# Kernel tuning notes

Hardware: AMD Instinct MI355X
Metric: run time of the kernel (lower is better)

## Reference

```python
import jax, jax.numpy as jnp
import numpy as np

NEG_NUM = -10000.0

def setup_inputs() -> dict:
    key = jax.random.key(0)
    k1, k2, k3, k4, k5, k6 = jax.random.split(key, 6)
    batch, enc_len = 32, 2048
    ctx_size, query_size, att_hid = 1024, 1024, 512
    in_dim = ctx_size + query_size
    ctx = jax.random.normal(k1, (batch, enc_len, ctx_size), dtype=jnp.float32)
    query = jax.random.normal(k2, (batch, query_size), dtype=jnp.float32)
    mask = jax.random.randint(k3, (batch, enc_len), 0, 2, dtype=jnp.int32)
    # Linear params (stored as (in, out) for x @ W + b)
    s1 = 1.0 / np.sqrt(in_dim)
    W1 = jax.random.uniform(k4, (in_dim, att_hid), jnp.float32, -s1, s1)
    b1 = jnp.zeros((att_hid,), jnp.float32)
    s2 = 1.0 / np.sqrt(att_hid)
    W2 = jax.random.uniform(k5, (att_hid, 1), jnp.float32, -s2, s2)
    b2 = jnp.zeros((1,), jnp.float32)
    return {"ctx": ctx, "query": query, "W1": W1, "b1": b1, "W2": W2, "b2": b2, "mask": mask}

def reference(ctx, query, W1, b1, W2, b2, mask):
    # ctx: (B, S, Dc), query: (B, Dq)
    B, S, Dc = ctx.shape
    Dq = query.shape[-1]
    # Equivalent to concat([ctx, query_expanded]) @ W1: split W1 into ctx/query blocks
    Wc, Wq = W1[:Dc], W1[Dc:]
    hidden = jnp.tanh(jnp.einsum('bsd,dh->bsh', ctx, Wc)
                      + (query @ Wq)[:, None, :] + b1)      # (B, S, H)
    score = jnp.einsum('bsh,h->bs', hidden, W2[:, 0]) + b2[0]  # (B, S)
    score = jnp.where(mask == 0, NEG_NUM, score)
    p_ctx = jax.nn.softmax(score, axis=-1)                   # (B, S)
    expected_ctx = jnp.einsum('bs,bsd->bd', p_ctx, ctx)      # (B, Dc)
    return (expected_ctx, p_ctx)
```

## Files before the change

kernel.cpp:

```cpp
#include <hip/hip_runtime.h>

typedef __bf16 bf16;
typedef __attribute__((ext_vector_type(8))) __bf16 bf16x8;
typedef __attribute__((ext_vector_type(4))) __bf16 bf16x4;
typedef __attribute__((ext_vector_type(4))) float f32x4;

#define B_  32
#define S_  2048
#define DC  1024
#define DQ  1024
#define H_  512
#define M_  (B_*S_)

#define BM  128
#define BN  512
#define BK  32

#define GLD16(g, l) __builtin_amdgcn_global_load_lds( \
    (__attribute__((address_space(1))) void*)(g),     \
    (__attribute__((address_space(3))) void*)(l), 16, 0, 0)

__global__ __launch_bounds__(256) void k_wconv(const float* __restrict__ W1,
                                               bf16* __restrict__ WcT2) {
    __shared__ bf16 t[32 * 520];
    const int kb = blockIdx.x, tid = threadIdx.x;
    #pragma unroll
    for (int i = 0; i < 16; ++i) {
        int base = (i * 256 + tid) * 4;
        int k = base >> 9;
        int h = base & 511;
        const float4 v = *(const float4*)(W1 + ((size_t)(kb * 32 + k)) * H_ + h);
        bf16x4 pk = { (bf16)v.x, (bf16)v.y, (bf16)v.z, (bf16)v.w };
        *(bf16x4*)(&t[k * 520 + h]) = pk;
    }
    __syncthreads();
    #pragma unroll
    for (int i = 0; i < 16; ++i) {
        int j = (i * 256 + tid) * 4;
        int col = j >> 5;
        int kk  = j & 31;
        bf16x4 o = { t[kk * 520 + col], t[(kk + 1) * 520 + col],
                     t[(kk + 2) * 520 + col], t[(kk + 3) * 520 + col] };
        *(bf16x4*)(WcT2 + (size_t)kb * 16384 + j) = o;
    }
}

__global__ __launch_bounds__(256) void k_qb(const float* __restrict__ query,
                                            const float* __restrict__ W1,
                                            const float* __restrict__ b1,
                                            float* __restrict__ qb) {
    const int hblk = blockIdx.x, b = blockIdx.y, tid = threadIdx.x;
    __shared__ float q[DQ];
    __shared__ float red[256];
    #pragma unroll
    for (int i = 0; i < 4; ++i)
        q[tid + i * 256] = query[(size_t)b * DQ + tid + i * 256];
    __syncthreads();
    const int h  = hblk * 64 + (tid & 63);
    const int kc = tid >> 6;
    const float* w = W1 + (size_t)DC * H_ + (size_t)(kc * 256) * H_ + h;
    const float* qv = q + kc * 256;
    float acc = 0.0f;
    #pragma unroll 8
    for (int k = 0; k < 256; ++k)
        acc = fmaf(qv[k], w[(size_t)k * H_], acc);
    red[tid] = acc;
    __syncthreads();
    if (tid < 64)
        qb[(size_t)b * H_ + hblk * 64 + tid] =
            red[tid] + red[tid + 64] + red[tid + 128] + red[tid + 192] + b1[hblk * 64 + tid];
}

__global__ __launch_bounds__(512, 2) void k_gemm(const float* __restrict__ ctx,
                                                 const bf16*  __restrict__ WcT2,
                                                 const float* __restrict__ qb,
                                                 const float* __restrict__ W2,
                                                 float* __restrict__ score) {
    __shared__ bf16 As[BM * BK];
    __shared__ bf16 Bs[BN * BK];
    __shared__ float qs[BN];
    __shared__ float ws2[BN];
    __shared__ float red[BM * 4];

    const int tid  = threadIdx.x;
    const int mblk = blockIdx.x;
    const size_t row_base = (size_t)mblk * BM;
    const int b = mblk >> 4;

    qs[tid]  = qb[(size_t)b * H_ + tid];
    ws2[tid] = W2[tid];

    const int lane = tid & 63;
    const int wave = tid >> 6;
    const int wm   = wave & 1;
    const int wn   = wave >> 1;
    const int l16  = lane & 15;
    const int quad = lane >> 4;

    f32x4 acc[4][8] = {};

    const int am = tid >> 2;
    const int ak = (tid & 3) << 3;
    const float* actx = ctx + (row_base + am) * (size_t)DC + ak;
    bf16* awr = &As[am * BK + ak];
    const bf16* bsrc = WcT2 + tid * 8;
    bf16* bdst = &Bs[tid * 8];
    const bf16* aP = &As[(wm * 64 + l16) * BK + quad * 8];
    const bf16* bP = &Bs[(wn * 128 + l16) * BK + quad * 8];

    for (int kb = 0; kb < DC / BK; ++kb) {
        #pragma unroll
        for (int i = 0; i < 4; ++i)
            GLD16(bsrc + (size_t)kb * 16384 + i * 4096, bdst + i * 4096);
        const float4 v0 = *(const float4*)(actx + kb * BK);
        const float4 v1 = *(const float4*)(actx + kb * BK + 4);
        bf16x8 a8 = { (bf16)v0.x, (bf16)v0.y, (bf16)v0.z, (bf16)v0.w,
                      (bf16)v1.x, (bf16)v1.y, (bf16)v1.z, (bf16)v1.w };
        *(bf16x8*)awr = a8;
        __syncthreads();

        bf16x8 aF[4], bF[8];
        #pragma unroll
        for (int mf = 0; mf < 4; ++mf) aF[mf] = *(const bf16x8*)(aP + mf * (16 * BK));
        #pragma unroll
        for (int nf = 0; nf < 8; ++nf) bF[nf] = *(const bf16x8*)(bP + nf * (16 * BK));
        #pragma unroll
        for (int mf = 0; mf < 4; ++mf)
            #pragma unroll
            for (int nf = 0; nf < 8; ++nf)
                acc[mf][nf] = __builtin_amdgcn_mfma_f32_16x16x32_bf16(aF[mf], bF[nf], acc[mf][nf], 0, 0, 0);
        __syncthreads();
    }

    float qv[8], wv[8];
    #pragma unroll
    for (int nf = 0; nf < 8; ++nf) {
        int c = wn * 128 + nf * 16 + l16;
        qv[nf] = qs[c];
        wv[nf] = ws2[c];
    }
    #pragma unroll
    for (int mf = 0; mf < 4; ++mf) {
        #pragma unroll
        for (int r = 0; r < 4; ++r) {
            float s = 0.0f;
            #pragma unroll
            for (int nf = 0; nf < 8; ++nf) {
                float x = acc[mf][nf][r] + qv[nf];
                float t = 1.0f - 2.0f / (1.0f + __expf(2.0f * x));
                s = fmaf(t, wv[nf], s);
            }
            s += __shfl_xor(s, 1);
            s += __shfl_xor(s, 2);
            s += __shfl_xor(s, 4);
            s += __shfl_xor(s, 8);
            if (l16 == 0)
                red[(wm * 64 + mf * 16 + quad * 4 + r) * 4 + wn] = s;
        }
    }
    __syncthreads();
    if (tid < BM)
        score[row_base + tid] = red[tid * 4] + red[tid * 4 + 1] + red[tid * 4 + 2] + red[tid * 4 + 3];
}

__global__ __launch_bounds__(256) void k_softmax(const float* __restrict__ score,
                                                 const float* __restrict__ b2,
                                                 const int*   __restrict__ mask,
                                                 float* __restrict__ p_out) {
    int b = blockIdx.x, tid = threadIdx.x;
    __shared__ float red[256];
    float loc[8];
    float b2v = b2[0];
    float mx = -1e30f;
    #pragma unroll
    for (int i = 0; i < 8; ++i) {
        size_t r = (size_t)b * S_ + i * 256 + tid;
        float v = score[r] + b2v;
        if (mask[r] == 0) v = -10000.0f;
        loc[i] = v;
        mx = fmaxf(mx, v);
    }
    red[tid] = mx; __syncthreads();
    for (int o = 128; o > 0; o >>= 1) {
        if (tid < o) red[tid] = fmaxf(red[tid], red[tid + o]);
        __syncthreads();
    }
    mx = red[0]; __syncthreads();
    float se = 0.0f;
    #pragma unroll
    for (int i = 0; i < 8; ++i) {
        float e = __expf(loc[i] - mx);
        loc[i] = e;
        se += e;
    }
    red[tid] = se; __syncthreads();
    for (int o = 128; o > 0; o >>= 1) {
        if (tid < o) red[tid] += red[tid + o];
        __syncthreads();
    }
    float inv = 1.0f / red[0];
    #pragma unroll
    for (int i = 0; i < 8; ++i)
        p_out[(size_t)b * S_ + i * 256 + tid] = loc[i] * inv;
}

__global__ __launch_bounds__(256) void k_expected(const float* __restrict__ ctx,
                                                  const float* __restrict__ p,
                                                  float* __restrict__ partial) {
    int b = blockIdx.x, ch = blockIdx.y, tid = threadIdx.x;
    __shared__ float ps[128];
    if (tid < 128) ps[tid] = p[(size_t)b * S_ + ch * 128 + tid];
    __syncthreads();
    const float* base = ctx + ((size_t)b * S_ + ch * 128) * DC + tid * 4;
    float ax = 0.f, ay = 0.f, az = 0.f, aw = 0.f;
    #pragma unroll 4
    for (int s = 0; s < 128; ++s) {
        const float4 v = *(const float4*)(base + (size_t)s * DC);
        float w = ps[s];
        ax = fmaf(w, v.x, ax);
        ay = fmaf(w, v.y, ay);
        az = fmaf(w, v.z, az);
        aw = fmaf(w, v.w, aw);
    }
    float4 o = { ax, ay, az, aw };
    *(float4*)(partial + ((size_t)(b * 16 + ch)) * DC + tid * 4) = o;
}

__global__ __launch_bounds__(256) void k_reduce(const float* __restrict__ partial,
                                                float* __restrict__ out) {
    int b = blockIdx.x, tid = threadIdx.x;
    float4 acc = { 0.f, 0.f, 0.f, 0.f };
    #pragma unroll
    for (int c = 0; c < 16; ++c) {
        const float4 v = *(const float4*)(partial + ((size_t)(b * 16 + c)) * DC + tid * 4);
        acc.x += v.x; acc.y += v.y; acc.z += v.z; acc.w += v.w;
    }
    *(float4*)(out + (size_t)b * DC + tid * 4) = acc;
}

extern "C" void kernel_launch(void* const* d_in, const int* in_sizes, int n_in,
                              void* d_out, int out_size, void* d_ws, size_t ws_size,
                              hipStream_t stream) {
    (void)in_sizes; (void)n_in; (void)out_size; (void)ws_size;
    const float* ctx   = (const float*)d_in[0];
    const float* query = (const float*)d_in[1];
    const float* W1    = (const float*)d_in[2];
    const float* b1    = (const float*)d_in[3];
    const float* W2    = (const float*)d_in[4];
    const float* b2    = (const float*)d_in[5];
    const int*   mask  = (const int*)d_in[6];

    float* out      = (float*)d_out;
    float* expected = out;
    float* p_out    = out + 32768;

    char* w = (char*)d_ws;
    bf16*  WcT2      = (bf16*)w;
    float* qb        = (float*)(w + (1 << 20));
    float* score     = (float*)(w + (1 << 20) + (64 << 10));
    float* partial_e = (float*)(w + (1 << 20) + (320 << 10));

    k_wconv   <<<32, 256, 0, stream>>>(W1, WcT2);
    k_qb      <<<dim3(8, B_), 256, 0, stream>>>(query, W1, b1, qb);
    k_gemm    <<<512, 512, 0, stream>>>(ctx, WcT2, qb, W2, score);
    k_softmax <<<B_, 256, 0, stream>>>(score, b2, mask, p_out);
    k_expected<<<dim3(B_, 16), 256, 0, stream>>>(ctx, p_out, partial_e);
    k_reduce  <<<B_, 256, 0, stream>>>(partial_e, expected);
}
```

Before: 521.0 us.

## Double-buffer GEMM tiles, merge prep kernels, split expected-ctx into more chunks

The GEMM main loop now double-buffers its A and B LDS tiles, prefetching the next K slice while MFMAs run on the current one, so only one barrier per iteration is needed. The weight conversion and query projection kernels are merged into one finer-grained prep launch. The expected-context pass is split into 32 chunks instead of 16 for more parallelism. Risks: 80KB of LDS per block lowers occupancy (launch bounds drop the min-2 hint), and the reduce step now sums twice as many partials.

```diff
diff --git a/kernel.cpp b/kernel.cpp
--- a/kernel.cpp
+++ b/kernel.cpp
@@ -15,80 +15,78 @@
 #define BM  128
 #define BN  512
 #define BK  32
+#define NCH 32
 
 #define GLD16(g, l) __builtin_amdgcn_global_load_lds( \
     (__attribute__((address_space(1))) void*)(g),     \
     (__attribute__((address_space(3))) void*)(l), 16, 0, 0)
 
-__global__ __launch_bounds__(256) void k_wconv(const float* __restrict__ W1,
-                                               bf16* __restrict__ WcT2) {
-    __shared__ bf16 t[32 * 520];
-    const int kb = blockIdx.x, tid = threadIdx.x;
-    #pragma unroll
-    for (int i = 0; i < 16; ++i) {
-        int base = (i * 256 + tid) * 4;
-        int k = base >> 9;
-        int h = base & 511;
-        const float4 v = *(const float4*)(W1 + ((size_t)(kb * 32 + k)) * H_ + h);
-        bf16x4 pk = { (bf16)v.x, (bf16)v.y, (bf16)v.z, (bf16)v.w };
-        *(bf16x4*)(&t[k * 520 + h]) = pk;
-    }
-    __syncthreads();
-    #pragma unroll
-    for (int i = 0; i < 16; ++i) {
-        int j = (i * 256 + tid) * 4;
-        int col = j >> 5;
-        int kk  = j & 31;
-        bf16x4 o = { t[kk * 520 + col], t[(kk + 1) * 520 + col],
-                     t[(kk + 2) * 520 + col], t[(kk + 3) * 520 + col] };
-        *(bf16x4*)(WcT2 + (size_t)kb * 16384 + j) = o;
-    }
-}
-
-__global__ __launch_bounds__(256) void k_qb(const float* __restrict__ query,
-                                            const float* __restrict__ W1,
-                                            const float* __restrict__ b1,
-                                            float* __restrict__ qb) {
-    const int hblk = blockIdx.x, b = blockIdx.y, tid = threadIdx.x;
-    __shared__ float q[DQ];
-    __shared__ float red[256];
-    #pragma unroll
-    for (int i = 0; i < 4; ++i)
-        q[tid + i * 256] = query[(size_t)b * DQ + tid + i * 256];
-    __syncthreads();
-    const int h  = hblk * 64 + (tid & 63);
-    const int kc = tid >> 6;
-    const float* w = W1 + (size_t)DC * H_ + (size_t)(kc * 256) * H_ + h;
-    const float* qv = q + kc * 256;
-    float acc = 0.0f;
-    #pragma unroll 8
-    for (int k = 0; k < 256; ++k)
-        acc = fmaf(qv[k], w[(size_t)k * H_], acc);
-    red[tid] = acc;
-    __syncthreads();
-    if (tid < 64)
-        qb[(size_t)b * H_ + hblk * 64 + tid] =
-            red[tid] + red[tid + 64] + red[tid + 128] + red[tid + 192] + b1[hblk * 64 + tid];
-}
-
-__global__ __launch_bounds__(512, 2) void k_gemm(const float* __restrict__ ctx,
-                                                 const bf16*  __restrict__ WcT2,
-                                                 const float* __restrict__ qb,
-                                                 const float* __restrict__ W2,
-                                                 float* __restrict__ score) {
-    __shared__ bf16 As[BM * BK];
-    __shared__ bf16 Bs[BN * BK];
-    __shared__ float qs[BN];
-    __shared__ float ws2[BN];
-    __shared__ float red[BM * 4];
+__global__ __launch_bounds__(256) void k_prep(const float* __restrict__ W1,
+                                              const float* __restrict__ query,
+                                              const float* __restrict__ b1,
+                                              bf16* __restrict__ WcT2,
+                                              float* __restrict__ qb) {
+    const int bid = blockIdx.x, tid = threadIdx.x;
+    if (bid < 256) {
+        __shared__ bf16 t[32 * 68];
+        const int kb = bid >> 3;
+        const int cb = bid & 7;
+        #pragma unroll
+        for (int i = 0; i < 2; ++i) {
+            int idx = i * 256 + tid;
+            int k  = idx >> 4;
+            int h4 = (idx & 15) * 4;
+            const float4 v = *(const float4*)(W1 + ((size_t)(kb * 32 + k)) * H_ + cb * 64 + h4);
+            bf16x4 pk = { (bf16)v.x, (bf16)v.y, (bf16)v.z, (bf16)v.w };
+            *(bf16x4*)(&t[k * 68 + h4]) = pk;
+        }
+        __syncthreads();
+        const int col = tid >> 2;
+        const int kk0 = (tid & 3) * 8;
+        bf16x8 o;
+        #pragma unroll
+        for (int j = 0; j < 8; ++j) o[j] = t[(kk0 + j) * 68 + col];
+        *(bf16x8*)(WcT2 + (size_t)kb * 16384 + (size_t)(cb * 64 + col) * 32 + kk0) = o;
+    } else {
+        const int r = bid - 256;
+        const int hblk = r & 7;
+        const int b    = r >> 3;
+        __shared__ float q[DQ];
+        __shared__ float red[256];
+        #pragma unroll
+        for (int i = 0; i < 4; ++i)
+            q[tid + i * 256] = query[(size_t)b * DQ + tid + i * 256];
+        __syncthreads();
+        const int h  = hblk * 64 + (tid & 63);
+        const int kc = tid >> 6;
+        const float* w = W1 + (size_t)DC * H_ + (size_t)(kc * 256) * H_ + h;
+        const float* qv = q + kc * 256;
+        float acc = 0.0f;
+        #pragma unroll 8
+        for (int k = 0; k < 256; ++k)
+            acc = fmaf(qv[k], w[(size_t)k * H_], acc);
+        red[tid] = acc;
+        __syncthreads();
+        if (tid < 64)
+            qb[(size_t)b * H_ + hblk * 64 + tid] =
+                red[tid] + red[tid + 64] + red[tid + 128] + red[tid + 192] + b1[hblk * 64 + tid];
+    }
+}
+
+__global__ __launch_bounds__(512) void k_gemm(const float* __restrict__ ctx,
+                                              const bf16*  __restrict__ WcT2,
+                                              const float* __restrict__ qb,
+                                              const float* __restrict__ W2,
+                                              float* __restrict__ score) {
+    __shared__ char smem_raw[81920];
+    bf16* As = (bf16*)smem_raw;
+    bf16* Bs = (bf16*)(smem_raw + 16384);
+    float* red = (float*)smem_raw;
 
     const int tid  = threadIdx.x;
     const int mblk = blockIdx.x;
     const size_t row_base = (size_t)mblk * BM;
     const int b = mblk >> 4;
-
-    qs[tid]  = qb[(size_t)b * H_ + tid];
-    ws2[tid] = W2[tid];
 
     const int lane = tid & 63;
     const int wave = tid >> 6;
@@ -102,24 +100,39 @@
     const int am = tid >> 2;
     const int ak = (tid & 3) << 3;
     const float* actx = ctx + (row_base + am) * (size_t)DC + ak;
-    bf16* awr = &As[am * BK + ak];
+    const int aoff = am * BK + ak;
     const bf16* bsrc = WcT2 + tid * 8;
-    bf16* bdst = &Bs[tid * 8];
-    const bf16* aP = &As[(wm * 64 + l16) * BK + quad * 8];
-    const bf16* bP = &Bs[(wn * 128 + l16) * BK + quad * 8];
-
-    for (int kb = 0; kb < DC / BK; ++kb) {
-        #pragma unroll
-        for (int i = 0; i < 4; ++i)
-            GLD16(bsrc + (size_t)kb * 16384 + i * 4096, bdst + i * 4096);
-        const float4 v0 = *(const float4*)(actx + kb * BK);
-        const float4 v1 = *(const float4*)(actx + kb * BK + 4);
+    const int boff = tid * 8;
+    const int fA = (wm * 64 + l16) * BK + quad * 8;
+    const int fB = (wn * 128 + l16) * BK + quad * 8;
+
+    {
+        const float4 v0 = *(const float4*)(actx);
+        const float4 v1 = *(const float4*)(actx + 4);
         bf16x8 a8 = { (bf16)v0.x, (bf16)v0.y, (bf16)v0.z, (bf16)v0.w,
                       (bf16)v1.x, (bf16)v1.y, (bf16)v1.z, (bf16)v1.w };
-        *(bf16x8*)awr = a8;
-        __syncthreads();
+        *(bf16x8*)(As + aoff) = a8;
+        #pragma unroll
+        for (int i = 0; i < 4; ++i)
+            GLD16(bsrc + i * 4096, Bs + boff + i * 4096);
+    }
+    __syncthreads();
+
+    for (int kb = 0; kb < DC / BK; ++kb) {
+        const int cur = kb & 1, nxt = cur ^ 1;
+        float4 av0, av1;
+        if (kb < 31) {
+            #pragma unroll
+            for (int i = 0; i < 4; ++i)
+                GLD16(bsrc + (size_t)(kb + 1) * 16384 + i * 4096,
+                      Bs + nxt * 16384 + boff + i * 4096);
+            av0 = *(const float4*)(actx + (kb + 1) * BK);
+            av1 = *(const float4*)(actx + (kb + 1) * BK + 4);
+        }
 
         bf16x8 aF[4], bF[8];
+        const bf16* aP = As + cur * 4096 + fA;
+        const bf16* bP = Bs + cur * 16384 + fB;
         #pragma unroll
         for (int mf = 0; mf < 4; ++mf) aF[mf] = *(const bf16x8*)(aP + mf * (16 * BK));
         #pragma unroll
@@ -129,6 +142,12 @@
             #pragma unroll
             for (int nf = 0; nf < 8; ++nf)
                 acc[mf][nf] = __builtin_amdgcn_mfma_f32_16x16x32_bf16(aF[mf], bF[nf], acc[mf][nf], 0, 0, 0);
+
+        if (kb < 31) {
+            bf16x8 a8 = { (bf16)av0.x, (bf16)av0.y, (bf16)av0.z, (bf16)av0.w,
+                          (bf16)av1.x, (bf16)av1.y, (bf16)av1.z, (bf16)av1.w };
+            *(bf16x8*)(As + nxt * 4096 + aoff) = a8;
+        }
         __syncthreads();
     }
 
@@ -136,8 +155,8 @@
     #pragma unroll
     for (int nf = 0; nf < 8; ++nf) {
         int c = wn * 128 + nf * 16 + l16;
-        qv[nf] = qs[c];
-        wv[nf] = ws2[c];
+        qv[nf] = qb[(size_t)b * H_ + c];
+        wv[nf] = W2[c];
     }
     #pragma unroll
     for (int mf = 0; mf < 4; ++mf) {
@@ -208,13 +227,13 @@
                                                   const float* __restrict__ p,
                                                   float* __restrict__ partial) {
     int b = blockIdx.x, ch = blockIdx.y, tid = threadIdx.x;
-    __shared__ float ps[128];
-    if (tid < 128) ps[tid] = p[(size_t)b * S_ + ch * 128 + tid];
+    __shared__ float ps[64];
+    if (tid < 64) ps[tid] = p[(size_t)b * S_ + ch * 64 + tid];
     __syncthreads();
-    const float* base = ctx + ((size_t)b * S_ + ch * 128) * DC + tid * 4;
+    const float* base = ctx + ((size_t)b * S_ + ch * 64) * DC + tid * 4;
     float ax = 0.f, ay = 0.f, az = 0.f, aw = 0.f;
-    #pragma unroll 4
-    for (int s = 0; s < 128; ++s) {
+    #pragma unroll 8
+    for (int s = 0; s < 64; ++s) {
         const float4 v = *(const float4*)(base + (size_t)s * DC);
         float w = ps[s];
         ax = fmaf(w, v.x, ax);
@@ -223,7 +242,7 @@
         aw = fmaf(w, v.w, aw);
     }
     float4 o = { ax, ay, az, aw };
-    *(float4*)(partial + ((size_t)(b * 16 + ch)) * DC + tid * 4) = o;
+    *(float4*)(partial + ((size_t)(b * NCH + ch)) * DC + tid * 4) = o;
 }
 
 __global__ __launch_bounds__(256) void k_reduce(const float* __restrict__ partial,
@@ -231,8 +250,8 @@
     int b = blockIdx.x, tid = threadIdx.x;
     float4 acc = { 0.f, 0.f, 0.f, 0.f };
     #pragma unroll
-    for (int c = 0; c < 16; ++c) {
-        const float4 v = *(const float4*)(partial + ((size_t)(b * 16 + c)) * DC + tid * 4);
+    for (int c = 0; c < NCH; ++c) {
+        const float4 v = *(const float4*)(partial + ((size_t)(b * NCH + c)) * DC + tid * 4);
         acc.x += v.x; acc.y += v.y; acc.z += v.z; acc.w += v.w;
     }
     *(float4*)(out + (size_t)b * DC + tid * 4) = acc;
@@ -260,10 +279,9 @@
     float* score     = (float*)(w + (1 << 20) + (64 << 10));
     float* partial_e = (float*)(w + (1 << 20) + (320 << 10));
 
-    k_wconv   <<<32, 256, 0, stream>>>(W1, WcT2);
-    k_qb      <<<dim3(8, B_), 256, 0, stream>>>(query, W1, b1, qb);
+    k_prep    <<<512, 256, 0, stream>>>(W1, query, b1, WcT2, qb);
     k_gemm    <<<512, 512, 0, stream>>>(ctx, WcT2, qb, W2, score);
     k_softmax <<<B_, 256, 0, stream>>>(score, b2, mask, p_out);
-    k_expected<<<dim3(B_, 16), 256, 0, stream>>>(ctx, p_out, partial_e);
+    k_expected<<<dim3(B_, NCH), 256, 0, stream>>>(ctx, p_out, partial_e);
     k_reduce  <<<B_, 256, 0, stream>>>(partial_e, expected);
 }
```

Measured after the change: 493.9 us. -5.2%, faster.
